# Kernel optimization log

Hardware: AMD Instinct MI355X
Metric: run time of the kernel (lower is better)

The kernel has to match this reference:

```python
import jax, jax.numpy as jnp
import numpy as np

T_, N_, DIN, D, HEADS, WW, E_, DPE = 8, 20000, 128, 128, 4, 4, 320000, 8
DH = D // HEADS
NEG = -1e30
EPS_GATE = 1e-6


def setup_inputs() -> dict:
    key = jax.random.key(0)
    ks = jax.random.split(key, 10)
    return {
        "H_tilde": jax.random.normal(ks[0], (T_, N_, DIN), jnp.float32),
        "S": jax.random.uniform(ks[1], (T_, N_), jnp.float32),
        "Wq": jax.random.normal(ks[2], (D, DIN), jnp.float32) * 0.05,
        "Wkh": jax.random.normal(ks[3], (D, DIN), jnp.float32) * 0.05,
        "Wkpe": jax.random.normal(ks[4], (D, DPE), jnp.float32) * 0.05,
        "Wv": jax.random.normal(ks[5], (D, DIN), jnp.float32) * 0.05,
        "pe_table": jax.random.normal(ks[6], (WW + 1, DPE), jnp.float32),
        "rel_bias": jax.random.normal(ks[7], (WW + 1,), jnp.float32),
        "src": jax.random.randint(ks[8], (E_,), 0, N_),
        "dst": jax.random.randint(ks[9], (E_,), 0, N_),
    }


def reference(H_tilde, S, Wq, Wkh, Wkpe, Wv, pe_table, rel_bias, src, dst):
    T, N, _ = H_tilde.shape
    H, dh, W = HEADS, DH, WW
    scale = dh ** -0.5
    dtype = H_tilde.dtype

    # Projections (torch Linear: x @ W.T). W_k over concat([H, pe]) splits additively.
    Q = (H_tilde @ Wq.T).reshape(T, N, H, dh)
    K0 = (H_tilde @ Wkh.T).reshape(T, N, H, dh)
    V = (H_tilde @ Wv.T).reshape(T, N, H, dh)
    pe_k = (pe_table @ Wkpe.T).reshape(W + 1, H, dh)
    gate = jnp.log(jnp.clip(S, 0.0, 1.0) + EPS_GATE)  # (T, N)

    # Pad W zero-steps in front so a length-(W+1) slice at t covers t-W..t.
    pad = lambda x: jnp.concatenate([jnp.zeros((W,) + x.shape[1:], x.dtype), x], axis=0)
    Kp, Vp, gp = pad(K0), pad(V), pad(gate)

    def step(_, tq):
        t, Qt = tq  # Qt: (N, H, dh)
        Kwin = jax.lax.dynamic_slice_in_dim(Kp, t, W + 1, 0)[::-1]  # (W+1,N,H,dh), dt=0..W
        Vwin = jax.lax.dynamic_slice_in_dim(Vp, t, W + 1, 0)[::-1]
        gwin = jax.lax.dynamic_slice_in_dim(gp, t, W + 1, 0)[::-1]  # (W+1, N)
        Qd = Qt[dst]  # (E, H, dh)

        scores = []
        for dt in range(W + 1):
            Ks = Kwin[dt][src] + pe_k[dt][None]  # (E, H, dh)
            s = (jnp.einsum('ehc,ehc->eh', Qd, Ks) * scale
                 + rel_bias[dt] + gwin[dt][src][:, None])
            scores.append(jnp.where(dt <= t, s, NEG))  # mask dt > t (W_eff = min(W, t))
        sc = jnp.stack(scores)  # (W+1, E, H)

        # Segment softmax over incoming edges of each dst node, jointly over dt.
        mx = jax.ops.segment_max(sc.transpose(1, 0, 2), dst, num_segments=N)  # (N,W+1,H)
        mx = mx.max(axis=1)  # (N, H)
        valid = (jnp.arange(W + 1) <= t)[:, None, None]
        ex = jnp.where(valid, jnp.exp(sc - mx[dst][None]), 0.0)  # (W+1, E, H)

        denom = jax.ops.segment_sum(ex.sum(axis=0), dst, num_segments=N)  # (N, H)
        numer = jnp.zeros((N, H, dh), dtype)
        for dt in range(W + 1):
            contrib = ex[dt][:, :, None] * Vwin[dt][src]  # (E, H, dh)
            numer = numer + jax.ops.segment_sum(contrib, dst, num_segments=N)

        msg = numer / jnp.maximum(denom, 1e-12)[:, :, None]  # (N, H, dh)
        return None, msg.reshape(N, H * dh)

    _, M_out = jax.lax.scan(step, None, (jnp.arange(T), Q))
    return M_out  # (T, N, d)
```

## Files before the change

### kernel.cpp

```cpp
#include <hip/hip_runtime.h>

typedef unsigned short u16;
typedef unsigned int u32;
typedef __attribute__((ext_vector_type(8))) __bf16 bf16x8;
typedef __attribute__((ext_vector_type(4))) float f32x4;
typedef __attribute__((ext_vector_type(4))) _Float16 f16x4;
typedef __attribute__((ext_vector_type(2))) unsigned u32x2;

constexpr int TT = 8, NN = 20000, DD = 128, EE = 320000;
constexpr int MAXDEG = 64;
constexpr float SCL = 0.17677669529663687f;
constexpr int VBLK2 = 544;
constexpr u32 SLAB = (u32)(NN * DD);

__device__ __forceinline__ u16 f2bf(float f) {
  return __builtin_bit_cast(u16, (__bf16)f);
}
__device__ __forceinline__ u16 f2h(float f) {
  return __builtin_bit_cast(u16, (_Float16)f);
}
__device__ __forceinline__ float blo(u32 u) { return __uint_as_float(u << 16); }
__device__ __forceinline__ float bhi(u32 u) { return __uint_as_float(u & 0xffff0000u); }

__device__ __forceinline__ bf16x8 cvt8(float4 f0, float4 f1) {
  bf16x8 r;
  r[0] = (__bf16)f0.x; r[1] = (__bf16)f0.y; r[2] = (__bf16)f0.z; r[3] = (__bf16)f0.w;
  r[4] = (__bf16)f1.x; r[5] = (__bf16)f1.y; r[6] = (__bf16)f1.z; r[7] = (__bf16)f1.w;
  return r;
}

__global__ void k_init(const float* __restrict__ pe_table, const float* __restrict__ Wkpe,
                       const float* __restrict__ Wq, const float* __restrict__ Wkh,
                       const float* __restrict__ Wv, const float* __restrict__ S,
                       float* __restrict__ pek, int* __restrict__ cnt,
                       u16* __restrict__ Wb, float* __restrict__ SgT) {
  int i = blockIdx.x * 256 + threadIdx.x;
  if (i < NN) cnt[i] = 0;
  if (i < 5 * DD) {
    int dt = i >> 7, j = i & 127;
    float s = 0.f;
    for (int p = 0; p < 8; ++p) s += pe_table[dt * 8 + p] * Wkpe[j * 8 + p];
    pek[i] = s;
  }
  if (i < 3 * DD * DD) {
    int y = i / (DD * DD), idx = i % (DD * DD);
    const float* W = (y == 0) ? Wq : (y == 1) ? Wkh : Wv;
    Wb[i] = f2bf(W[idx]);
  }
  if (i < TT * NN) {
    SgT[i] = fminf(fmaxf(S[i], 0.f), 1.f) + 1e-6f;
  }
}

__global__ void k_build(const int* __restrict__ src, const int* __restrict__ dst,
                        int* __restrict__ cnt, int* __restrict__ eslot) {
  int i = blockIdx.x * 256 + threadIdx.x;
  if (i < EE) {
    int d = dst[i];
    int p = atomicAdd(&cnt[d], 1);
    if (p < MAXDEG) eslot[d * MAXDEG + p] = src[i];
  }
}

__global__ __launch_bounds__(256) void k_proj6(
    const float* __restrict__ Hm, const u16* __restrict__ Wb,
    u16* __restrict__ Qb, u16* __restrict__ Kb, u16* __restrict__ Vb) {
  int tid = threadIdx.x;
  int lane = tid & 63, wv = tid >> 6;
  int wr = wv >> 1, wc = wv & 1;
  int l15 = lane & 15, lq = lane >> 4;
  size_t m0 = (size_t)blockIdx.x * 128;

  bf16x8 a[4][4];
#pragma unroll
  for (int ks = 0; ks < 4; ++ks) {
    int col0 = ks * 32 + lq * 8;
#pragma unroll
    for (int i = 0; i < 4; ++i) {
      const float* gp = Hm + (m0 + wr * 64 + i * 16 + l15) * DD + col0;
      a[ks][i] = cvt8(*(const float4*)gp, *(const float4*)(gp + 4));
    }
  }

  for (int y = 0; y < 3; ++y) {
    u16* Out = (y == 0) ? Qb : (y == 1) ? Kb : Vb;
    const bool asF16 = (y == 2);
    const float postm = (y == 0) ? SCL : 1.f;
    const u16* Wy = Wb + y * DD * DD;

    f32x4 acc[4][4];
    for (int i = 0; i < 4; ++i)
      for (int j = 0; j < 4; ++j) acc[i][j] = (f32x4){0.f, 0.f, 0.f, 0.f};

    for (int ks = 0; ks < 4; ++ks) {
      int col0 = ks * 32 + lq * 8;
      bf16x8 b[4];
#pragma unroll
      for (int j = 0; j < 4; ++j)
        b[j] = *(const bf16x8*)(Wy + (wc * 64 + j * 16 + l15) * DD + col0);
#pragma unroll
      for (int i = 0; i < 4; ++i)
#pragma unroll
        for (int j = 0; j < 4; ++j)
          acc[i][j] = __builtin_amdgcn_mfma_f32_16x16x32_bf16(a[ks][i], b[j], acc[i][j], 0, 0, 0);
    }

#pragma unroll
    for (int i = 0; i < 4; ++i)
#pragma unroll
      for (int j = 0; j < 4; ++j)
#pragma unroll
        for (int g = 0; g < 4; ++g) {
          size_t row = m0 + wr * 64 + i * 16 + lq * 4 + g;
          int col = wc * 64 + j * 16 + l15;
          float v = acc[i][j][g] * postm;
          Out[row * DD + col] = asF16 ? f2h(v) : f2bf(v);
        }
  }
}

__global__ __launch_bounds__(256, 8) void k_agg14(
    const u16* __restrict__ Qb, const u16* __restrict__ Kb, const u16* __restrict__ Vb,
    const float* __restrict__ SgT, const float* __restrict__ pek,
    const float* __restrict__ relb,
    const int* __restrict__ cnt, const int* __restrict__ eslot,
    float* __restrict__ outp) {
  __shared__ int srcB[MAXDEG];
  __shared__ float gateS[TT][MAXDEG];
  __shared__ float eW[4][TT][16];
  __shared__ u16 VldsS[4][VBLK2];
  int tid = threadIdx.x;
  const int h = tid >> 6, lane = tid & 63;
  const int n = blockIdx.x;

  int deg = min(cnt[n], MAXDEG);
  if (tid < MAXDEG) {
    int s = (tid < deg) ? eslot[n * MAXDEG + tid] : 0;
    srcB[tid] = s * DD;
  }
  for (int i = tid; i < TT * MAXDEG; i += 256) {
    int tp = i >> 6, e = i & 63;
    float g = 0.f;
    if (e < deg) g = SgT[(size_t)tp * NN + eslot[n * MAXDEG + e]];
    gateS[tp][e] = g;
  }

  const int t16 = lane & 15, qo = lane >> 4, qo4 = qo * 4;
  const int h32 = h * 32;

  uint4 qb;
  {
    bool qok = t16 < 8;
    const u16* Qp = Qb + ((size_t)(t16 & 7) * NN + n) * DD + h32 + qo * 8;
    qb = qok ? *(const uint4*)(Qp) : make_uint4(0u, 0u, 0u, 0u);
  }

  {
    ((float*)&eW[h][0][0])[lane] = -1e30f;
    ((float*)&eW[h][0][0])[lane + 64] = -1e30f;
    float qf0 = blo(qb.x), qf1 = bhi(qb.x), qf2 = blo(qb.y), qf3 = bhi(qb.y);
    float qf4 = blo(qb.z), qf5 = bhi(qb.z), qf6 = blo(qb.w), qf7 = bhi(qb.w);
#pragma unroll
    for (int d = 0; d < 5; ++d) {
      const float* pp = pek + d * DD + h32 + qo * 8;
      float4 p0 = *(const float4*)pp;
      float4 p1 = *(const float4*)(pp + 4);
      float s = qf0 * p0.x + qf1 * p0.y + qf2 * p0.z + qf3 * p0.w
              + qf4 * p1.x + qf5 * p1.y + qf6 * p1.z + qf7 * p1.w;
      s += __shfl_xor(s, 16);
      s += __shfl_xor(s, 32);
      int tp = t16 - d;
      if (qo == 0 && t16 < 8 && tp >= 0) eW[h][tp][t16] = s + relb[d];
    }
  }
  __syncthreads();

  f32x4 num0 = (f32x4){0.f, 0.f, 0.f, 0.f};
  f32x4 num1 = (f32x4){0.f, 0.f, 0.f, 0.f};
  float dd = 0.f;

  if (deg > 0) {
    const int degm1 = deg - 1;
    const int nch = (deg + 15) >> 4;
    const int cmax = nch << 4;
    const int nj = nch * 8;

    const int vkey = lane >> 2, vcb = lane & 3;
    u16* vbuf = &VldsS[h][0];
    unsigned trbase = (unsigned)(uintptr_t)vbuf + lane * 8;
    unsigned woff = (unsigned)((vcb >> 1) * VBLK2 + (vkey >> 2) * 128 +
                               (vkey & 3) * 32 + (vcb & 1) * 16);
    const float* eWt = &eW[h][0][t16];
    const u32 kbase = (u32)(h32 + qo * 8);
    const u32 vbase = (u32)(h32 + vcb * 8);

    auto loadK = [&](u32 koff, int c16) -> uint4 {
      u32 idx = koff + (u32)srcB[min(c16 + t16, degm1)] + kbase;
      return *(const uint4*)(Kb + idx);
    };
    auto loadV = [&](u32 koff, int c16) -> uint4 {
      u32 idx = koff + (u32)srcB[min(c16 + vkey, degm1)] + vbase;
      return *(const uint4*)(Vb + idx);
    };
    auto writeV = [&](uint4 f) { *(uint4*)((char*)vbuf + woff) = f; };
    auto compute = [&](uint4 ka, int tp, int c16) {
      float Lf = eWt[tp * 16];
      f32x4 g4 = *(const f32x4*)&gateS[tp][c16 + qo4];

      f32x4 z = (f32x4){0.f, 0.f, 0.f, 0.f};
      f32x4 sc = __builtin_amdgcn_mfma_f32_16x16x32_bf16(
          __builtin_bit_cast(bf16x8, ka), __builtin_bit_cast(bf16x8, qb), z, 0, 0, 0);

      float w0 = __expf(sc[0] + Lf) * g4[0];
      float w1 = __expf(sc[1] + Lf) * g4[1];
      float w2 = __expf(sc[2] + Lf) * g4[2];
      float w3 = __expf(sc[3] + Lf) * g4[3];
      dd += w0 + w1 + w2 + w3;
      u32x2 wpk;
      wpk.x = __builtin_bit_cast(u32, __builtin_amdgcn_cvt_pkrtz(w0, w1));
      wpk.y = __builtin_bit_cast(u32, __builtin_amdgcn_cvt_pkrtz(w2, w3));
      f16x4 wf = __builtin_bit_cast(f16x4, wpk);

      __builtin_amdgcn_sched_barrier(0);
      u32x2 vr0, vr1;
      asm volatile("ds_read_b64_tr_b16 %0, %1" : "=v"(vr0) : "v"(trbase));
      asm volatile("ds_read_b64_tr_b16 %0, %1 offset:544" : "=v"(vr1) : "v"(trbase));
      asm volatile("s_waitcnt lgkmcnt(0)");
      __builtin_amdgcn_sched_barrier(0);
      num0 = __builtin_amdgcn_mfma_f32_16x16x16f16(
          wf, __builtin_bit_cast(f16x4, vr0), num0, 0, 0, 0);
      num1 = __builtin_amdgcn_mfma_f32_16x16x16f16(
          wf, __builtin_bit_cast(f16x4, vr1), num1, 0, 0, 0);
    };

    uint4 kA = loadK(0u, 0);
    { uint4 v0 = loadV(0u, 0); writeV(v0); }
    int tp0 = 0, c0 = 0;
    int tp1 = 0, c1 = 16;
    u32 koff1 = 0u;
    if (c1 >= cmax) { c1 = 0; tp1 = 1; koff1 = SLAB; }
    uint4 kB = loadK(koff1, c1);
    uint4 vB = loadV(koff1, c1);
    int tpn = tp1, cn = c1;
    u32 koffn = koff1;
    cn += 16; if (cn >= cmax) { cn = 0; ++tpn; koffn += SLAB; }

    for (int j = 0; j < nj; ++j) {
      bool more2 = (j + 2) < nj;
      uint4 kC = make_uint4(0u, 0u, 0u, 0u), vC = make_uint4(0u, 0u, 0u, 0u);
      if (more2) {
        kC = loadK(koffn, cn);
        vC = loadV(koffn, cn);
      }
      compute(kA, tp0, c0);
      __builtin_amdgcn_sched_barrier(0);
      if ((j + 1) < nj) writeV(vB);
      kA = kB; kB = kC; vB = vC;
      tp0 = tp1; c0 = c1;
      tp1 = tpn; c1 = cn;
      cn += 16; if (cn >= cmax) { cn = 0; ++tpn; koffn += SLAB; }
    }
  }

  float Dh = dd;
  Dh += __shfl_xor(Dh, 16);
  Dh += __shfl_xor(Dh, 32);
#pragma unroll
  for (int r = 0; r < 4; ++r) {
    int t = qo4 + r;
    float Dt = __shfl(Dh, t);
    if (t < 8) {
      float inv = 1.f / fmaxf(Dt, 1e-12f);
      float* op = outp + ((size_t)t * NN + n) * DD + h32;
      op[t16] = num0[r] * inv;
      op[16 + t16] = num1[r] * inv;
    }
  }
}

extern "C" void kernel_launch(void* const* d_in, const int* in_sizes, int n_in,
                              void* d_out, int out_size, void* d_ws, size_t ws_size,
                              hipStream_t stream) {
  const float* Hm = (const float*)d_in[0];
  const float* S = (const float*)d_in[1];
  const float* Wq = (const float*)d_in[2];
  const float* Wkh = (const float*)d_in[3];
  const float* Wkpe = (const float*)d_in[4];
  const float* Wv = (const float*)d_in[5];
  const float* pe_table = (const float*)d_in[6];
  const float* relb = (const float*)d_in[7];
  const int* src = (const int*)d_in[8];
  const int* dst = (const int*)d_in[9];
  float* out = (float*)d_out;

  auto aup = [](size_t x) { return (x + 255) & ~(size_t)255; };
  char* base = (char*)d_ws;
  size_t off = 0;
  u16* Qb = (u16*)(base + off); off = aup(off + (size_t)TT * NN * DD * 2);
  u16* Kb = (u16*)(base + off); off = aup(off + (size_t)TT * NN * DD * 2);
  u16* Vb = (u16*)(base + off); off = aup(off + (size_t)TT * NN * DD * 2);
  float* pek = (float*)(base + off); off = aup(off + (size_t)5 * DD * 4);
  float* SgT = (float*)(base + off); off = aup(off + (size_t)TT * NN * 4);
  int* cnt = (int*)(base + off); off = aup(off + (size_t)NN * 4);
  int* eslot = (int*)(base + off); off = aup(off + (size_t)NN * MAXDEG * 4);
  u16* Wb = (u16*)(base + off); off = aup(off + (size_t)3 * DD * DD * 2);
  (void)ws_size; (void)in_sizes; (void)n_in; (void)out_size;

  k_init<<<(TT * NN + 255) / 256, 256, 0, stream>>>(pe_table, Wkpe, Wq, Wkh, Wv, S,
                                                    pek, cnt, Wb, SgT);
  k_build<<<(EE + 255) / 256, 256, 0, stream>>>(src, dst, cnt, eslot);
  k_proj6<<<1250, 256, 0, stream>>>(Hm, Wb, Qb, Kb, Vb);
  k_agg14<<<NN, 256, 0, stream>>>(Qb, Kb, Vb, SgT, pek, relb, cnt, eslot, out);
}
```

Baseline: 299.9 us.

## Flatten (timestep, edge) pairs to remove per-timestep chunk padding in aggregation

The aggregation kernel previously handled each of the 8 source timesteps in 16-edge chunks padded to the next multiple of 16, so low-degree nodes wasted many MFMA lanes on padding. It now builds a flat list of (timestep, edge) pairs in shared memory, with precomputed K/V offsets and the timestep index packed into the low bits of the gate value. Chunks of 16 can then span timesteps, which reduces the number of iterations. In exchange, each lane does per-element LDS lookups of the bias term, an integer divide during setup, and sees slightly perturbed gate values.

```diff
diff --git a/kernel.cpp b/kernel.cpp
--- a/kernel.cpp
+++ b/kernel.cpp
@@ -119,14 +119,14 @@
   }
 }
 
-__global__ __launch_bounds__(256, 8) void k_agg14(
+__global__ __launch_bounds__(256, 8) void k_agg15(
     const u16* __restrict__ Qb, const u16* __restrict__ Kb, const u16* __restrict__ Vb,
     const float* __restrict__ SgT, const float* __restrict__ pek,
     const float* __restrict__ relb,
     const int* __restrict__ cnt, const int* __restrict__ eslot,
     float* __restrict__ outp) {
-  __shared__ int srcB[MAXDEG];
-  __shared__ float gateS[TT][MAXDEG];
+  __shared__ u32 offF[TT * MAXDEG];
+  __shared__ float gateF[TT * MAXDEG];
   __shared__ float eW[4][TT][16];
   __shared__ u16 VldsS[4][VBLK2];
   int tid = threadIdx.x;
@@ -134,15 +134,19 @@
   const int n = blockIdx.x;
 
   int deg = min(cnt[n], MAXDEG);
-  if (tid < MAXDEG) {
-    int s = (tid < deg) ? eslot[n * MAXDEG + tid] : 0;
-    srcB[tid] = s * DD;
-  }
+  const int extTot = deg * TT;
   for (int i = tid; i < TT * MAXDEG; i += 256) {
-    int tp = i >> 6, e = i & 63;
+    u32 eoff = 0u, tp = 0u;
     float g = 0.f;
-    if (e < deg) g = SgT[(size_t)tp * NN + eslot[n * MAXDEG + e]];
-    gateS[tp][e] = g;
+    if (i < extTot) {
+      tp = (u32)i / (u32)deg;
+      u32 key = (u32)i - tp * (u32)deg;
+      int s = eslot[n * MAXDEG + (int)key];
+      eoff = tp * SLAB + (u32)(s * DD);
+      g = SgT[(size_t)tp * NN + s];
+    }
+    offF[i] = eoff;
+    gateF[i] = __uint_as_float((__float_as_uint(g) & ~7u) | tp);
   }
 
   const int t16 = lane & 15, qo = lane >> 4, qo4 = qo * 4;
@@ -180,41 +184,46 @@
   float dd = 0.f;
 
   if (deg > 0) {
-    const int degm1 = deg - 1;
-    const int nch = (deg + 15) >> 4;
-    const int cmax = nch << 4;
-    const int nj = nch * 8;
+    const int cmax = (extTot + 15) & ~15;
+    const int nj = cmax >> 4;
 
     const int vkey = lane >> 2, vcb = lane & 3;
     u16* vbuf = &VldsS[h][0];
     unsigned trbase = (unsigned)(uintptr_t)vbuf + lane * 8;
     unsigned woff = (unsigned)((vcb >> 1) * VBLK2 + (vkey >> 2) * 128 +
                                (vkey & 3) * 32 + (vcb & 1) * 16);
-    const float* eWt = &eW[h][0][t16];
+    const float* eWh = (const float*)&eW[h][0][0];
     const u32 kbase = (u32)(h32 + qo * 8);
     const u32 vbase = (u32)(h32 + vcb * 8);
 
-    auto loadK = [&](u32 koff, int c16) -> uint4 {
-      u32 idx = koff + (u32)srcB[min(c16 + t16, degm1)] + kbase;
+    auto loadK = [&](int c) -> uint4 {
+      u32 idx = offF[c + t16] + kbase;
       return *(const uint4*)(Kb + idx);
     };
-    auto loadV = [&](u32 koff, int c16) -> uint4 {
-      u32 idx = koff + (u32)srcB[min(c16 + vkey, degm1)] + vbase;
+    auto loadV = [&](int c) -> uint4 {
+      u32 idx = offF[c + vkey] + vbase;
       return *(const uint4*)(Vb + idx);
     };
     auto writeV = [&](uint4 f) { *(uint4*)((char*)vbuf + woff) = f; };
-    auto compute = [&](uint4 ka, int tp, int c16) {
-      float Lf = eWt[tp * 16];
-      f32x4 g4 = *(const f32x4*)&gateS[tp][c16 + qo4];
+    auto compute = [&](uint4 ka, int c) {
+      f32x4 g4 = *(const f32x4*)&gateF[c + qo4];
+      u32 tp0 = __float_as_uint(g4[0]) & 7u;
+      u32 tp1 = __float_as_uint(g4[1]) & 7u;
+      u32 tp2 = __float_as_uint(g4[2]) & 7u;
+      u32 tp3 = __float_as_uint(g4[3]) & 7u;
+      float Lf0 = eWh[tp0 * 16 + t16];
+      float Lf1 = eWh[tp1 * 16 + t16];
+      float Lf2 = eWh[tp2 * 16 + t16];
+      float Lf3 = eWh[tp3 * 16 + t16];
 
       f32x4 z = (f32x4){0.f, 0.f, 0.f, 0.f};
       f32x4 sc = __builtin_amdgcn_mfma_f32_16x16x32_bf16(
           __builtin_bit_cast(bf16x8, ka), __builtin_bit_cast(bf16x8, qb), z, 0, 0, 0);
 
-      float w0 = __expf(sc[0] + Lf) * g4[0];
-      float w1 = __expf(sc[1] + Lf) * g4[1];
-      float w2 = __expf(sc[2] + Lf) * g4[2];
-      float w3 = __expf(sc[3] + Lf) * g4[3];
+      float w0 = __expf(sc[0] + Lf0) * g4[0];
+      float w1 = __expf(sc[1] + Lf1) * g4[1];
+      float w2 = __expf(sc[2] + Lf2) * g4[2];
+      float w3 = __expf(sc[3] + Lf3) * g4[3];
       dd += w0 + w1 + w2 + w3;
       u32x2 wpk;
       wpk.x = __builtin_bit_cast(u32, __builtin_amdgcn_cvt_pkrtz(w0, w1));
@@ -233,32 +242,20 @@
           wf, __builtin_bit_cast(f16x4, vr1), num1, 0, 0, 0);
     };
 
-    uint4 kA = loadK(0u, 0);
-    { uint4 v0 = loadV(0u, 0); writeV(v0); }
-    int tp0 = 0, c0 = 0;
-    int tp1 = 0, c1 = 16;
-    u32 koff1 = 0u;
-    if (c1 >= cmax) { c1 = 0; tp1 = 1; koff1 = SLAB; }
-    uint4 kB = loadK(koff1, c1);
-    uint4 vB = loadV(koff1, c1);
-    int tpn = tp1, cn = c1;
-    u32 koffn = koff1;
-    cn += 16; if (cn >= cmax) { cn = 0; ++tpn; koffn += SLAB; }
+    uint4 kA = loadK(0);
+    { uint4 v0 = loadV(0); writeV(v0); }
+    uint4 kB = make_uint4(0u, 0u, 0u, 0u), vB = make_uint4(0u, 0u, 0u, 0u);
+    if (nj > 1) { kB = loadK(16); vB = loadV(16); }
+    int c0 = 0, c1 = 16, cn = 32;
 
     for (int j = 0; j < nj; ++j) {
-      bool more2 = (j + 2) < nj;
       uint4 kC = make_uint4(0u, 0u, 0u, 0u), vC = make_uint4(0u, 0u, 0u, 0u);
-      if (more2) {
-        kC = loadK(koffn, cn);
-        vC = loadV(koffn, cn);
-      }
-      compute(kA, tp0, c0);
+      if (cn < cmax) { kC = loadK(cn); vC = loadV(cn); }
+      compute(kA, c0);
       __builtin_amdgcn_sched_barrier(0);
-      if ((j + 1) < nj) writeV(vB);
+      if (c1 < cmax) writeV(vB);
       kA = kB; kB = kC; vB = vC;
-      tp0 = tp1; c0 = c1;
-      tp1 = tpn; c1 = cn;
-      cn += 16; if (cn >= cmax) { cn = 0; ++tpn; koffn += SLAB; }
+      c0 = c1; c1 = cn; cn += 16;
     }
   }
 
@@ -310,5 +307,5 @@
                                                     pek, cnt, Wb, SgT);
   k_build<<<(EE + 255) / 256, 256, 0, stream>>>(src, dst, cnt, eslot);
   k_proj6<<<1250, 256, 0, stream>>>(Hm, Wb, Qb, Kb, Vb);
-  k_agg14<<<NN, 256, 0, stream>>>(Qb, Kb, Vb, SgT, pek, relb, cnt, eslot, out);
-}
+  k_agg15<<<NN, 256, 0, stream>>>(Qb, Kb, Vb, SgT, pek, relb, cnt, eslot, out);
+}
```

New measurement: 302.2 us. No clear change (+0.8%).
